# Optimization experiments

Measured on AMD Instinct MI355X. Metric: run time of the kernel, lower is better.

## Reference

```python
import jax, jax.numpy as jnp
import numpy as np

N_NODES = 50000

def cheb_conv(x, edge_index, W, b):
    # PyG ChebConv, K=2, normalization='sym', lambda_max=2.0 (default):
    # scaled Laplacian L_hat = (2/lambda_max)*L - I = -D^{-1/2} A D^{-1/2} (zero diag).
    # Tx_0 = x, Tx_1 = L_hat @ x ; out = Tx_0 @ W[0] + Tx_1 @ W[1] + b
    src, dst = edge_index[0], edge_index[1]
    ones = jnp.ones(src.shape[0], x.dtype)
    deg = jax.ops.segment_sum(ones, src, num_segments=N_NODES)
    dinv = jnp.where(deg > 0, 1.0 / jnp.sqrt(deg), 0.0)
    norm = -dinv[src] * dinv[dst]                                   # [E]
    tx1 = jax.ops.segment_sum(x[src] * norm[:, None], dst, num_segments=N_NODES)
    return x @ W[0] + tx1 @ W[1] + b

def setup_inputs() -> dict:
    key = jax.random.key(0)
    ks = jax.random.split(key, 12)
    IN, OUT, E, P = 128, 2, 800000, 400000
    return {
        "x": jax.random.normal(ks[0], (N_NODES, IN), jnp.float32),
        "edge_index": jax.random.randint(ks[1], (2, E), 0, N_NODES),
        "E_pos": jax.random.randint(ks[2], (2, P), 0, N_NODES),
        "neg_edge_index": jax.random.randint(ks[3], (2, P), 0, N_NODES),
        "W1": jax.random.normal(ks[4], (2, IN, 300), jnp.float32) * 0.05,
        "b1": jnp.zeros((300,), jnp.float32),
        "W2": jax.random.normal(ks[5], (2, 300, 100), jnp.float32) * 0.05,
        "b2": jnp.zeros((100,), jnp.float32),
        "W3": jax.random.normal(ks[6], (2, 100, OUT), jnp.float32) * 0.05,
        "b3": jnp.zeros((OUT,), jnp.float32),
        "lin1_W": jax.random.normal(ks[7], (100, IN), jnp.float32) * 0.05,
        "lin1_b": jnp.zeros((100,), jnp.float32),
        "lin2_W": jax.random.normal(ks[8], (100, IN), jnp.float32) * 0.05,
        "lin2_b": jnp.zeros((100,), jnp.float32),
        "c1": jnp.full((1,), 0.5, jnp.float32),
        "c2": jnp.full((1,), 0.5, jnp.float32),
    }

def reference(x, edge_index, E_pos, neg_edge_index, W1, b1, W2, b2, W3, b3,
              lin1_W, lin1_b, lin2_W, lin2_b, c1, c2):
    # eval mode: F.dropout and dropout_edge are identity
    x0 = x
    h = jax.nn.relu(cheb_conv(x0, edge_index, W1, b1))
    x1 = jax.nn.relu(cheb_conv(h, edge_index, W2, b2))
    x2 = x1 + jax.nn.relu(x0 @ lin1_W.T + lin1_b)
    z = x1 + jax.nn.relu(x0 @ lin2_W.T + lin2_b)
    pos_score = jnp.sum(z[E_pos[0]] * z[E_pos[1]], axis=1)              # [P]
    pos_loss = -jnp.mean(jnp.log(jax.nn.sigmoid(pos_score) + 1e-15))
    neg_score = jnp.sum(z[neg_edge_index[0]] * z[neg_edge_index[1]], axis=1)
    neg_loss = -jnp.mean(jnp.log(1.0 - jax.nn.sigmoid(neg_score) + 1e-15))
    r_loss = pos_loss + neg_loss
    out = cheb_conv(x2, edge_index, W3, b3)                             # [N, out_channels]
    return (out, r_loss, c1, c2)
```

## Files before the change

kernel.cpp:

```cpp
#include <hip/hip_runtime.h>
#include <math.h>


typedef unsigned short ushort_t;
typedef unsigned char u8;
typedef __attribute__((ext_vector_type(8))) __bf16 bf16x8;
typedef __attribute__((ext_vector_type(8))) short s16x8;
typedef __attribute__((ext_vector_type(4))) float f32x4;
typedef __attribute__((ext_vector_type(2))) float f32x2;

#define NB_H 64
#define HW 12500
#define PW 25000

__device__ __forceinline__ f32x4 mfma16x16x32(s16x8 a, s16x8 b, f32x4 c) {
  return __builtin_amdgcn_mfma_f32_16x16x32_bf16(
      __builtin_bit_cast(bf16x8, a), __builtin_bit_cast(bf16x8, b), c, 0, 0, 0);
}
__device__ __forceinline__ ushort_t f2bf(float f) {
  union { float f; unsigned u; } c; c.f = f;
  unsigned r = (c.u + 0x7FFFu + ((c.u >> 16) & 1u)) >> 16;
  return (ushort_t)r;
}
__device__ __forceinline__ f32x2 cvt2lo(unsigned u) {
  return __builtin_amdgcn_cvt_pk_f32_fp8((int)u, false);
}
__device__ __forceinline__ f32x2 cvt2hi(unsigned u) {
  return __builtin_amdgcn_cvt_pk_f32_fp8((int)u, true);
}
__device__ __forceinline__ u8 f2fp8(float f) {
  return (u8)(__builtin_amdgcn_cvt_pk_fp8_f32(f, 0.f, 0, false) & 0xff);
}

template<int VAR, int NT, int KTOT>
__global__ __launch_bounds__(256) void gemm_mfma(
    const ushort_t* __restrict__ A0, const ushort_t* __restrict__ A1,
    const ushort_t* __restrict__ Wt,
    const float* __restrict__ bias0, const float* __restrict__ bias1,
    const float* __restrict__ x1,
    const float* __restrict__ W3c, const float* __restrict__ b3c,
    void* __restrict__ out0, void* __restrict__ out1,
    float* __restrict__ t0g, float* __restrict__ t1g, int M)
{
  constexpr int NF = NT / 32;
  __shared__ __align__(16) ushort_t As[64 * 40];
  __shared__ __align__(16) ushort_t Bs[NT * 40];
  __shared__ float w3s[400];
  const int tid  = threadIdx.x;
  const int lane = tid & 63, w = tid >> 6;
  const int m0 = blockIdx.x * 64;
  const int wm = (w & 1) * 32, wn = (w >> 1) * (NT / 2);
  if (VAR == 2) { for (int i = tid; i < 400; i += 256) w3s[i] = W3c[i]; }
  f32x4 acc[2][NF];
#pragma unroll
  for (int i = 0; i < 2; ++i)
#pragma unroll
    for (int j = 0; j < NF; ++j) acc[i][j] = (f32x4){0.f, 0.f, 0.f, 0.f};

  for (int k0 = 0; k0 < KTOT; k0 += 32) {
    {
      const int r = tid >> 2, c8 = (tid & 3) * 8;
      const int gm = m0 + r;
      uint4 v = {0u, 0u, 0u, 0u};
      if (gm < M) {
        if (VAR == 1) {
          const u8* s8 = (const u8*)A0 + (size_t)gm * 320 + k0 + c8;
          const uint2 r8 = *(const uint2*)s8;
          const f32x2 f0 = cvt2lo(r8.x), f1 = cvt2hi(r8.x);
          const f32x2 f2 = cvt2lo(r8.y), f3 = cvt2hi(r8.y);
          v.x = (unsigned)f2bf(f0.x) | ((unsigned)f2bf(f0.y) << 16);
          v.y = (unsigned)f2bf(f1.x) | ((unsigned)f2bf(f1.y) << 16);
          v.z = (unsigned)f2bf(f2.x) | ((unsigned)f2bf(f2.y) << 16);
          v.w = (unsigned)f2bf(f3.x) | ((unsigned)f2bf(f3.y) << 16);
        } else {
          const ushort_t* srcp;
          if (VAR == 0) srcp = (k0 < 128) ? A0 + (size_t)gm * 128 + k0 + c8
                                          : A1 + (size_t)gm * 128 + (k0 - 128) + c8;
          else srcp = A0 + (size_t)gm * 128 + k0 + c8;
          v = *(const uint4*)srcp;
        }
      }
      *(uint4*)&As[r * 40 + c8] = v;
    }
    {
      const int c8 = (tid & 3) * 8;
#pragma unroll
      for (int i = 0; i < (NT * 4 + 255) / 256; ++i) {
        const int r = (tid >> 2) + i * 64;
        if (r < NT)
          *(uint4*)&Bs[r * 40 + c8] = *(const uint4*)(Wt + (size_t)r * KTOT + k0 + c8);
      }
    }
    __syncthreads();
    s16x8 af[2], bfr[NF];
#pragma unroll
    for (int mi = 0; mi < 2; ++mi)
      af[mi] = *(const s16x8*)&As[(wm + mi * 16 + (lane & 15)) * 40 + (lane >> 4) * 8];
#pragma unroll
    for (int ni = 0; ni < NF; ++ni)
      bfr[ni] = *(const s16x8*)&Bs[(wn + ni * 16 + (lane & 15)) * 40 + (lane >> 4) * 8];
#pragma unroll
    for (int mi = 0; mi < 2; ++mi)
#pragma unroll
      for (int ni = 0; ni < NF; ++ni)
        acc[mi][ni] = mfma16x16x32(af[mi], bfr[ni], acc[mi][ni]);
    __syncthreads();
  }

  if (VAR == 2) {
#pragma unroll
    for (int mi = 0; mi < 2; ++mi)
#pragma unroll
      for (int r = 0; r < 4; ++r) {
        const int gRow = m0 + wm + mi * 16 + ((lane >> 4) << 2) + r;
        float p0 = 0.f, p1 = 0.f, p2 = 0.f, p3 = 0.f;
#pragma unroll
        for (int ni = 0; ni < NF; ++ni) {
          const int col = wn + ni * 16 + (lane & 15);
          const float v = acc[mi][ni][r];
          if (gRow < M) {
            if (col < 100) {
              const float x2v = x1[(size_t)gRow * 128 + col] + fmaxf(v + bias0[col], 0.f);
              p0 = fmaf(x2v, w3s[col * 2 + 0], p0);
              p1 = fmaf(x2v, w3s[col * 2 + 1], p1);
              p2 = fmaf(x2v, w3s[200 + col * 2 + 0], p2);
              p3 = fmaf(x2v, w3s[200 + col * 2 + 1], p3);
            } else if (col < 200) {
              const int c = col - 100;
              ((u8*)out1)[(size_t)gRow * 128 + c] =
                  f2fp8(x1[(size_t)gRow * 128 + c] + fmaxf(v + bias1[c], 0.f));
            }
          }
        }
        if (wn == 0) {
#pragma unroll
          for (int off = 8; off; off >>= 1) {
            p0 += __shfl_down(p0, off, 16);
            p1 += __shfl_down(p1, off, 16);
            p2 += __shfl_down(p2, off, 16);
            p3 += __shfl_down(p3, off, 16);
          }
          if ((lane & 15) == 0 && gRow < M) {
            t0g[(size_t)gRow * 2 + 0] = p0 + b3c[0];
            t0g[(size_t)gRow * 2 + 1] = p1 + b3c[1];
            t1g[(size_t)gRow * 2 + 0] = p2;
            t1g[(size_t)gRow * 2 + 1] = p3;
          }
        }
      }
  } else {
#pragma unroll
    for (int mi = 0; mi < 2; ++mi)
#pragma unroll
      for (int ni = 0; ni < NF; ++ni)
#pragma unroll
        for (int r = 0; r < 4; ++r) {
          const int gRow = m0 + wm + mi * 16 + ((lane >> 4) << 2) + r;
          const int col  = wn + ni * 16 + (lane & 15);
          if (gRow >= M) continue;
          const float v = acc[mi][ni][r];
          if (VAR == 0) {
            ((u8*)out0)[(size_t)gRow * 320 + col] =
                (col < 300) ? f2fp8(fmaxf(v + bias0[col], 0.f)) : (u8)0;
          } else {
            if (col < 100) ((float*)out0)[(size_t)gRow * 128 + col] = v + bias0[col];
            else if (col < 200) ((u8*)out1)[(size_t)gRow * 128 + (col - 100)] = f2fp8(v);
          }
        }
  }
}

__global__ __launch_bounds__(256) void prep(
    const int* __restrict__ src, const int* __restrict__ dst, int E, int M,
    unsigned* __restrict__ partS, unsigned* __restrict__ partD,
    ushort_t* __restrict__ rank,
    const int* __restrict__ ep, const int* __restrict__ en, int P,
    unsigned* __restrict__ partP, ushort_t* __restrict__ prank,
    const float* __restrict__ x, ushort_t* __restrict__ xb,
    u8* __restrict__ xf8, int n4,
    const float* __restrict__ W1, const float* __restrict__ W2,
    const float* __restrict__ l1W, const float* __restrict__ l2W,
    ushort_t* __restrict__ W1t, ushort_t* __restrict__ W2t,
    ushort_t* __restrict__ Wlt)
{
  __shared__ unsigned hist[HW];
  const int blk = blockIdx.x;
  if (blk < 2 * NB_H) {
    const int isD = (blk >= NB_H);
    const int b = isD ? blk - NB_H : blk;
    const int* keys = isD ? dst : src;
    unsigned* part = isD ? partD : partS;
    const int cs = (E + NB_H - 1) / NB_H;
    const int e0 = b * cs;
    const int e1 = (e0 + cs < E) ? e0 + cs : E;
    for (int r = 0; r < 2; ++r) {
      const int klo = r * 2 * HW;
      for (int i = threadIdx.x; i < HW; i += 256) hist[i] = 0;
      __syncthreads();
      for (int e = e0 + threadIdx.x; e < e1; e += 256) {
        const int k = keys[e] - klo;
        if ((unsigned)k < (unsigned)(2 * HW)) {
          const unsigned old = atomicAdd(&hist[k >> 1], (k & 1) ? 0x10000u : 1u);
          if (isD) rank[e] = (ushort_t)((old >> ((k & 1) * 16)) & 0xffffu);
        }
      }
      __syncthreads();
      for (int i = threadIdx.x; i < HW; i += 256)
        part[(size_t)b * PW + r * HW + i] = hist[i];
      __syncthreads();
    }
    return;
  }
  if (blk < 3 * NB_H) {
    const int b = blk - 2 * NB_H;
    const int twoP = 2 * P;
    const int cs2 = (twoP + NB_H - 1) / NB_H;
    const int e0 = b * cs2;
    const int e1 = (e0 + cs2 < twoP) ? e0 + cs2 : twoP;
    for (int r = 0; r < 2; ++r) {
      const int klo = r * 2 * HW;
      for (int i = threadIdx.x; i < HW; i += 256) hist[i] = 0;
      __syncthreads();
      for (int i = e0 + threadIdx.x; i < e1; i += 256) {
        const int neg = (i >= P);
        const int p = neg ? i - P : i;
        const int* ia = neg ? en : ep;
        const int k = ia[p] - klo;
        if ((unsigned)k < (unsigned)(2 * HW)) {
          const unsigned old = atomicAdd(&hist[k >> 1], (k & 1) ? 0x10000u : 1u);
          prank[i] = (ushort_t)((old >> ((k & 1) * 16)) & 0xffffu);
        }
      }
      __syncthreads();
      for (int i = threadIdx.x; i < HW; i += 256)
        partP[(size_t)b * PW + r * HW + i] = hist[i];
      __syncthreads();
    }
    return;
  }
  const int i = (blk - 3 * NB_H) * 256 + threadIdx.x;
  if (i < n4) {
    const float4 v = ((const float4*)x)[i];
    ushort4 o; o.x = f2bf(v.x); o.y = f2bf(v.y); o.z = f2bf(v.z); o.w = f2bf(v.w);
    ((ushort4*)xb)[i] = o;
    int p = 0;
    p = __builtin_amdgcn_cvt_pk_fp8_f32(v.x, v.y, p, false);
    p = __builtin_amdgcn_cvt_pk_fp8_f32(v.z, v.w, p, true);
    ((unsigned*)xf8)[i] = (unsigned)p;
    return;
  }
  const int j = i - n4;
  if (j < 81920) {
    const int n = j >> 8, k = j & 255;
    float v = 0.f;
    if (n < 300) v = (k < 128) ? W1[k * 300 + n] : W1[38400 + (k - 128) * 300 + n];
    W1t[j] = f2bf(v);
  } else if (j < 153600) {
    const int jj = j - 81920;
    const int n = jj / 320, k = jj - n * 320;
    float v = 0.f;
    if (n < 200 && k < 300) v = W2[(n < 100 ? 0 : 30000) + k * 100 + (n % 100)];
    W2t[jj] = f2bf(v);
  } else if (j < 182272) {
    const int jj = j - 153600;
    const int n = jj >> 7, k = jj & 127;
    float v = 0.f;
    if (n < 100) v = l1W[n * 128 + k];
    else if (n < 200) v = l2W[(n - 100) * 128 + k];
    Wlt[jj] = f2bf(v);
  }
}

__global__ void scan_local(const unsigned* __restrict__ partS,
                           unsigned* __restrict__ partD,
                           unsigned* __restrict__ partP,
                           float* __restrict__ dinv,
                           int* __restrict__ ptr, int* __restrict__ pptr,
                           int* __restrict__ bsumE, int* __restrict__ bsumP, int n)
{
  __shared__ int tmp[256];
  const int i = blockIdx.x * 256 + threadIdx.x;
  const int lane = threadIdx.x & 63;
  unsigned ssum = 0, dtot = 0, ptot = 0;
  if (i < n && (i & 1) == 0) {
    const int c = i >> 1;
    for (int b = 0; b < NB_H; b += 8) {
      unsigned sv[8];
#pragma unroll
      for (int q = 0; q < 8; ++q) sv[q] = partS[(size_t)(b + q) * PW + c];
#pragma unroll
      for (int q = 0; q < 8; ++q) ssum += sv[q];
    }
    unsigned run = 0;
    for (int b = 0; b < NB_H; b += 8) {
      unsigned dv[8];
#pragma unroll
      for (int q = 0; q < 8; ++q) dv[q] = partD[(size_t)(b + q) * PW + c];
#pragma unroll
      for (int q = 0; q < 8; ++q) { const unsigned pre = run; run += dv[q]; dv[q] = pre; }
#pragma unroll
      for (int q = 0; q < 8; ++q) partD[(size_t)(b + q) * PW + c] = dv[q];
    }
    dtot = run;
    unsigned prun = 0;
    for (int b = 0; b < NB_H; b += 8) {
      unsigned pv[8];
#pragma unroll
      for (int q = 0; q < 8; ++q) pv[q] = partP[(size_t)(b + q) * PW + c];
#pragma unroll
      for (int q = 0; q < 8; ++q) { const unsigned pre = prun; prun += pv[q]; pv[q] = pre; }
#pragma unroll
      for (int q = 0; q < 8; ++q) partP[(size_t)(b + q) * PW + c] = pv[q];
    }
    ptot = prun;
  }
  const unsigned sAll = __shfl(ssum, lane & ~1, 64);
  const unsigned dAll = __shfl(dtot, lane & ~1, 64);
  const unsigned pAll = __shfl(ptot, lane & ~1, 64);
  int v = 0, v2 = 0;
  if (i < n) {
    const int hs = (i & 1) * 16;
    const unsigned dg = (sAll >> hs) & 0xffffu;
    dinv[i] = dg ? 1.f / sqrtf((float)dg) : 0.f;
    v = (int)((dAll >> hs) & 0xffffu);
    v2 = (int)((pAll >> hs) & 0xffffu);
  }
  tmp[threadIdx.x] = v;
  __syncthreads();
  for (int off = 1; off < 256; off <<= 1) {
    const int t = (threadIdx.x >= off) ? tmp[threadIdx.x - off] : 0;
    __syncthreads();
    tmp[threadIdx.x] += t;
    __syncthreads();
  }
  if (i < n) ptr[i] = tmp[threadIdx.x] - v;
  if (threadIdx.x == 255) bsumE[blockIdx.x] = tmp[255];
  __syncthreads();
  tmp[threadIdx.x] = v2;
  __syncthreads();
  for (int off = 1; off < 256; off <<= 1) {
    const int t = (threadIdx.x >= off) ? tmp[threadIdx.x - off] : 0;
    __syncthreads();
    tmp[threadIdx.x] += t;
    __syncthreads();
  }
  if (i < n) pptr[i] = tmp[threadIdx.x] - v2;
  if (threadIdx.x == 255) bsumP[blockIdx.x] = tmp[255];
}

__global__ void scan_add2(int* __restrict__ ptr, int* __restrict__ pptr,
                          const int* __restrict__ bsumE, const int* __restrict__ bsumP,
                          int n, int E, int twoP, int nb, float* __restrict__ accs)
{
  __shared__ int tmp[256];
  const int v = (threadIdx.x < nb) ? bsumE[threadIdx.x] : 0;
  tmp[threadIdx.x] = v;
  __syncthreads();
  for (int off = 1; off < 256; off <<= 1) {
    const int t = (threadIdx.x >= off) ? tmp[threadIdx.x - off] : 0;
    __syncthreads();
    tmp[threadIdx.x] += t;
    __syncthreads();
  }
  const int offE = (blockIdx.x > 0) ? tmp[blockIdx.x - 1] : 0;
  __syncthreads();
  const int v2 = (threadIdx.x < nb) ? bsumP[threadIdx.x] : 0;
  tmp[threadIdx.x] = v2;
  __syncthreads();
  for (int off = 1; off < 256; off <<= 1) {
    const int t = (threadIdx.x >= off) ? tmp[threadIdx.x - off] : 0;
    __syncthreads();
    tmp[threadIdx.x] += t;
    __syncthreads();
  }
  const int offP = (blockIdx.x > 0) ? tmp[blockIdx.x - 1] : 0;
  const int i = blockIdx.x * 256 + threadIdx.x;
  if (i < n) { ptr[i] += offE; pptr[i] += offP; }
  if (i == 0) { ptr[n] = E; pptr[n] = twoP; accs[0] = 0.f; accs[1] = 0.f; }
}

__global__ __launch_bounds__(256) void fill2(
    const int* __restrict__ src, const int* __restrict__ dst,
    const float* __restrict__ dinv, const int* __restrict__ ptr,
    const unsigned* __restrict__ baseD, const ushort_t* __restrict__ rank,
    int2* __restrict__ csr, int E, int fillE,
    const int* __restrict__ ep, const int* __restrict__ en, int P,
    const int* __restrict__ pptr, const unsigned* __restrict__ baseP,
    const ushort_t* __restrict__ prank, int* __restrict__ pnb)
{
  const int blk = blockIdx.x;
  if (blk < fillE) {
    const int e = blk * 256 + threadIdx.x;
    if (e >= E) return;
    const int cs = (E + NB_H - 1) / NB_H;
    const int b = e / cs;
    const int s = src[e], d = dst[e];
    const unsigned bv = baseD[(size_t)b * PW + (d >> 1)];
    const int base = (int)((bv >> ((d & 1) * 16)) & 0xffffu);
    const int pos = ptr[d] + base + (int)rank[e];
    const float w = -dinv[s] * dinv[d];
    csr[pos] = make_int2(s, __float_as_int(w));
    return;
  }
  const int i = (blk - fillE) * 256 + threadIdx.x;
  const int twoP = 2 * P;
  if (i >= twoP) return;
  const int neg = (i >= P);
  const int p = neg ? i - P : i;
  const int* ia = neg ? en : ep;
  const int na = ia[p], nbv = ia[P + p];
  const int cs2 = (twoP + NB_H - 1) / NB_H;
  const int b = i / cs2;
  const unsigned bv = baseP[(size_t)b * PW + (na >> 1)];
  const int base = (int)((bv >> ((na & 1) * 16)) & 0xffffu);
  const int pos = pptr[na] + base + (int)prank[i];
  pnb[pos] = nbv | (neg ? (int)0x80000000 : 0);
}

#define ACCV(u, ww) { f32x2 t; \
  t = cvt2lo(u.x); a[0]  = fmaf(ww, t.x, a[0]);  a[1]  = fmaf(ww, t.y, a[1]);  \
  t = cvt2hi(u.x); a[2]  = fmaf(ww, t.x, a[2]);  a[3]  = fmaf(ww, t.y, a[3]);  \
  t = cvt2lo(u.y); a[4]  = fmaf(ww, t.x, a[4]);  a[5]  = fmaf(ww, t.y, a[5]);  \
  t = cvt2hi(u.y); a[6]  = fmaf(ww, t.x, a[6]);  a[7]  = fmaf(ww, t.y, a[7]);  \
  t = cvt2lo(u.z); a[8]  = fmaf(ww, t.x, a[8]);  a[9]  = fmaf(ww, t.y, a[9]);  \
  t = cvt2hi(u.z); a[10] = fmaf(ww, t.x, a[10]); a[11] = fmaf(ww, t.y, a[11]); \
  t = cvt2lo(u.w); a[12] = fmaf(ww, t.x, a[12]); a[13] = fmaf(ww, t.y, a[13]); \
  t = cvt2hi(u.w); a[14] = fmaf(ww, t.x, a[14]); a[15] = fmaf(ww, t.y, a[15]); }

__global__ __launch_bounds__(256) void gather128e(
    const u8* __restrict__ xf8, ushort_t* __restrict__ txb,
    const int* __restrict__ ptr, const int2* __restrict__ csr, int M)
{
  const int node = (blockIdx.x * 256 + threadIdx.x) >> 3;
  const int sub  = threadIdx.x & 7;
  if (node >= M) return;
  const int beg = ptr[node], end = ptr[node + 1];
  float a[16] = {};
  int p = beg;
  for (; p + 8 <= end; p += 8) {
    int2 e[8];
#pragma unroll
    for (int q = 0; q < 8; ++q) e[q] = csr[p + q];
    uint4 v[8];
#pragma unroll
    for (int q = 0; q < 8; ++q)
      v[q] = *(const uint4*)(xf8 + (size_t)e[q].x * 128 + sub * 16);
#pragma unroll
    for (int q = 0; q < 8; ++q) { const float wq = __int_as_float(e[q].y); ACCV(v[q], wq) }
  }
  for (; p < end; ++p) {
    const int2 eq = csr[p]; const float wq = __int_as_float(eq.y);
    const uint4 v = *(const uint4*)(xf8 + (size_t)eq.x * 128 + sub * 16);
    ACCV(v, wq)
  }
  uint4 o1, o2;
  o1.x = (unsigned)f2bf(a[0])  | ((unsigned)f2bf(a[1])  << 16);
  o1.y = (unsigned)f2bf(a[2])  | ((unsigned)f2bf(a[3])  << 16);
  o1.z = (unsigned)f2bf(a[4])  | ((unsigned)f2bf(a[5])  << 16);
  o1.w = (unsigned)f2bf(a[6])  | ((unsigned)f2bf(a[7])  << 16);
  o2.x = (unsigned)f2bf(a[8])  | ((unsigned)f2bf(a[9])  << 16);
  o2.y = (unsigned)f2bf(a[10]) | ((unsigned)f2bf(a[11]) << 16);
  o2.z = (unsigned)f2bf(a[12]) | ((unsigned)f2bf(a[13]) << 16);
  o2.w = (unsigned)f2bf(a[14]) | ((unsigned)f2bf(a[15]) << 16);
  ushort_t* dstp = txb + (size_t)node * 128 + sub * 16;
  *(uint4*)dstp = o1;
  *(uint4*)(dstp + 8) = o2;
}

__global__ __launch_bounds__(256) void gather100e_x1(
    const u8* __restrict__ Brh, float* __restrict__ Ar,
    const int* __restrict__ ptr, const int2* __restrict__ csr, int M)
{
  const int node = (blockIdx.x * 256 + threadIdx.x) >> 3;
  const int sub  = threadIdx.x & 7;
  if (node >= M) return;
  const int beg = ptr[node], end = ptr[node + 1];
  float a[16] = {};
  int p = beg;
  for (; p + 8 <= end; p += 8) {
    int2 e[8];
#pragma unroll
    for (int q = 0; q < 8; ++q) e[q] = csr[p + q];
    uint4 v[8];
#pragma unroll
    for (int q = 0; q < 8; ++q)
      v[q] = *(const uint4*)(Brh + (size_t)e[q].x * 128 + sub * 16);
#pragma unroll
    for (int q = 0; q < 8; ++q) { const float wq = __int_as_float(e[q].y); ACCV(v[q], wq) }
  }
  for (; p < end; ++p) {
    const int2 eq = csr[p]; const float wq = __int_as_float(eq.y);
    const uint4 v = *(const uint4*)(Brh + (size_t)eq.x * 128 + sub * 16);
    ACCV(v, wq)
  }
  float* dstp = Ar + (size_t)node * 128 + sub * 16;
#pragma unroll
  for (int q = 0; q < 4; ++q) {
    float4 b = *(const float4*)(dstp + q * 4);
    b.x = fmaxf(b.x + a[q * 4 + 0], 0.f);
    b.y = fmaxf(b.y + a[q * 4 + 1], 0.f);
    b.z = fmaxf(b.z + a[q * 4 + 2], 0.f);
    b.w = fmaxf(b.w + a[q * 4 + 3], 0.f);
    *(float4*)(dstp + q * 4) = b;
  }
}
#undef ACCV

__device__ __forceinline__ void maskrow(uint4& r, int sub) {
  if (sub >= 6) { r.y = 0u; r.z = 0u; r.w = 0u; if (sub == 7) r.x = 0u; }
}
#define DOTA(vv, s) { f32x2 q_; \
  q_ = cvt2lo(vv.x); s = fmaf(af[0],  q_.x, s); s = fmaf(af[1],  q_.y, s); \
  q_ = cvt2hi(vv.x); s = fmaf(af[2],  q_.x, s); s = fmaf(af[3],  q_.y, s); \
  q_ = cvt2lo(vv.y); s = fmaf(af[4],  q_.x, s); s = fmaf(af[5],  q_.y, s); \
  q_ = cvt2hi(vv.y); s = fmaf(af[6],  q_.x, s); s = fmaf(af[7],  q_.y, s); \
  q_ = cvt2lo(vv.z); s = fmaf(af[8],  q_.x, s); s = fmaf(af[9],  q_.y, s); \
  q_ = cvt2hi(vv.z); s = fmaf(af[10], q_.x, s); s = fmaf(af[11], q_.y, s); \
  q_ = cvt2lo(vv.w); s = fmaf(af[12], q_.x, s); s = fmaf(af[13], q_.y, s); \
  q_ = cvt2hi(vv.w); s = fmaf(af[14], q_.x, s); s = fmaf(af[15], q_.y, s); }

__global__ __launch_bounds__(256) void loss_g2(
    const u8* __restrict__ zf8, const int* __restrict__ pptr,
    const int* __restrict__ pnb, float* __restrict__ acc,
    const float* __restrict__ t1, const float* __restrict__ t0,
    const int* __restrict__ ptr, const int2* __restrict__ csr,
    float* __restrict__ out, int M, int lossNB)
{
  const int tid = threadIdx.x;
  if (blockIdx.x >= lossNB) {
    const int i = (blockIdx.x - lossNB) * 256 + tid;
    if (i >= M) return;
    float a0 = 0.f, a1 = 0.f;
    const int beg = ptr[i], end = ptr[i + 1];
    int p = beg;
    for (; p + 4 <= end; p += 4) {
      const int2 e0 = csr[p], e1 = csr[p + 1], e2 = csr[p + 2], e3 = csr[p + 3];
      const float w0 = __int_as_float(e0.y), w1 = __int_as_float(e1.y);
      const float w2 = __int_as_float(e2.y), w3 = __int_as_float(e3.y);
      const float2 v0 = *(const float2*)(t1 + (size_t)e0.x * 2);
      const float2 v1 = *(const float2*)(t1 + (size_t)e1.x * 2);
      const float2 v2 = *(const float2*)(t1 + (size_t)e2.x * 2);
      const float2 v3 = *(const float2*)(t1 + (size_t)e3.x * 2);
      a0 = fmaf(w0, v0.x, a0); a1 = fmaf(w0, v0.y, a1);
      a0 = fmaf(w1, v1.x, a0); a1 = fmaf(w1, v1.y, a1);
      a0 = fmaf(w2, v2.x, a0); a1 = fmaf(w2, v2.y, a1);
      a0 = fmaf(w3, v3.x, a0); a1 = fmaf(w3, v3.y, a1);
    }
    for (; p < end; ++p) {
      const int2 eq = csr[p]; const float wq = __int_as_float(eq.y);
      const float2 v = *(const float2*)(t1 + (size_t)eq.x * 2);
      a0 = fmaf(wq, v.x, a0); a1 = fmaf(wq, v.y, a1);
    }
    const float2 base = *(const float2*)(t0 + (size_t)i * 2);
    *(float2*)(out + (size_t)i * 2) = make_float2(base.x + a0, base.y + a1);
    return;
  }
  __shared__ float red[8];
  const int lane = tid & 63, wib = tid >> 6;
  const int sub = tid & 7;
  const int node = (blockIdx.x * 256 + tid) >> 3;
  float tp = 0.f, tn = 0.f;
  if (node < M) {
    uint4 ra = make_uint4(0u, 0u, 0u, 0u);
    if (sub < 7) ra = *(const uint4*)(zf8 + (size_t)node * 128 + sub * 16);
    maskrow(ra, sub);
    float af[16];
    { f32x2 t;
      t = cvt2lo(ra.x); af[0]  = t.x; af[1]  = t.y;
      t = cvt2hi(ra.x); af[2]  = t.x; af[3]  = t.y;
      t = cvt2lo(ra.y); af[4]  = t.x; af[5]  = t.y;
      t = cvt2hi(ra.y); af[6]  = t.x; af[7]  = t.y;
      t = cvt2lo(ra.z); af[8]  = t.x; af[9]  = t.y;
      t = cvt2hi(ra.z); af[10] = t.x; af[11] = t.y;
      t = cvt2lo(ra.w); af[12] = t.x; af[13] = t.y;
      t = cvt2hi(ra.w); af[14] = t.x; af[15] = t.y; }
    const int beg = pptr[node], end = pptr[node + 1];
    int p = beg;
    for (; p + 4 <= end; p += 4) {
      int nb4[4];
#pragma unroll
      for (int q = 0; q < 4; ++q) nb4[q] = pnb[p + q];
      uint4 rb[4];
#pragma unroll
      for (int q = 0; q < 4; ++q) {
        rb[q] = make_uint4(0u, 0u, 0u, 0u);
        const int nv = nb4[q] & 0x7fffffff;
        if (sub < 7) rb[q] = *(const uint4*)(zf8 + (size_t)nv * 128 + sub * 16);
        maskrow(rb[q], sub);
      }
      float s[4] = {0.f, 0.f, 0.f, 0.f};
#pragma unroll
      for (int q = 0; q < 4; ++q) DOTA(rb[q], s[q])
#pragma unroll
      for (int off = 4; off; off >>= 1) {
#pragma unroll
        for (int q = 0; q < 4; ++q) s[q] += __shfl_down(s[q], off, 8);
      }
      if (sub == 0) {
#pragma unroll
        for (int q = 0; q < 4; ++q) {
          const float sig = 1.f / (1.f + __expf(-s[q]));
          if ((unsigned)nb4[q] >> 31) tn += __logf(1.f - sig + 1e-15f);
          else tp += __logf(sig + 1e-15f);
        }
      }
    }
    for (; p < end; ++p) {
      const int nbv = pnb[p];
      const int nv = nbv & 0x7fffffff;
      uint4 rb = make_uint4(0u, 0u, 0u, 0u);
      if (sub < 7) rb = *(const uint4*)(zf8 + (size_t)nv * 128 + sub * 16);
      maskrow(rb, sub);
      float s = 0.f;
      DOTA(rb, s)
#pragma unroll
      for (int off = 4; off; off >>= 1) s += __shfl_down(s, off, 8);
      if (sub == 0) {
        const float sig = 1.f / (1.f + __expf(-s));
        if ((unsigned)nbv >> 31) tn += __logf(1.f - sig + 1e-15f);
        else tp += __logf(sig + 1e-15f);
      }
    }
  }
  tp += __shfl_down(tp, 32, 64); tn += __shfl_down(tn, 32, 64);
  tp += __shfl_down(tp, 16, 64); tn += __shfl_down(tn, 16, 64);
  tp += __shfl_down(tp, 8, 64);  tn += __shfl_down(tn, 8, 64);
  if (lane == 0) { red[wib] = tp; red[4 + wib] = tn; }
  __syncthreads();
  if (tid == 0) {
    atomicAdd(acc + 0, red[0] + red[1] + red[2] + red[3]);
    atomicAdd(acc + 1, red[4] + red[5] + red[6] + red[7]);
  }
}
#undef DOTA

__global__ void final_scalars(const float* __restrict__ accs,
                              const float* __restrict__ c1, const float* __restrict__ c2,
                              float* __restrict__ out, int M, float invP)
{
  out[2 * M + 0] = -(accs[0] + accs[1]) * invP;
  out[2 * M + 1] = c1[0];
  out[2 * M + 2] = c2[0];
}

extern "C" void kernel_launch(void* const* d_in, const int* in_sizes, int n_in,
                              void* d_out, int out_size, void* d_ws, size_t ws_size,
                              hipStream_t stream)
{
  const float* x   = (const float*)d_in[0];
  const int*   ei  = (const int*)d_in[1];
  const int*   ep  = (const int*)d_in[2];
  const int*   en  = (const int*)d_in[3];
  const float* W1  = (const float*)d_in[4];
  const float* b1  = (const float*)d_in[5];
  const float* W2  = (const float*)d_in[6];
  const float* b2  = (const float*)d_in[7];
  const float* W3  = (const float*)d_in[8];
  const float* b3  = (const float*)d_in[9];
  const float* l1W = (const float*)d_in[10];
  const float* l1b = (const float*)d_in[11];
  const float* l2W = (const float*)d_in[12];
  const float* l2b = (const float*)d_in[13];
  const float* c1  = (const float*)d_in[14];
  const float* c2  = (const float*)d_in[15];
  float* out = (float*)d_out;

  const int M = in_sizes[0] / 128;
  const int E = in_sizes[1] / 2;
  const int P = in_sizes[2] / 2;
  const int* src = ei;
  const int* dst = ei + E;
  const int nb_scan = (M + 255) / 256;
  const int fillE = (E + 255) / 256;
  const int fillP = (2 * P + 255) / 256;
  const int lossNB = (M * 8 + 255) / 256;

  float* ws = (float*)d_ws;
  size_t o = 0;
  float*    dinv = ws + o;            o += 50176;
  int*      ptr  = (int*)(ws + o);    o += (size_t)M + 8;
  int*      pptr = (int*)(ws + o);    o += (size_t)M + 8;
  int*      bsumE = (int*)(ws + o);   o += 256;
  int*      bsumP = (int*)(ws + o);   o += 256;
  int2*     csr  = (int2*)(ws + o);   o += (size_t)E * 2;
  ushort_t* rank = (ushort_t*)(ws + o); o += (size_t)E / 2;
  int*      pnb  = (int*)(ws + o);    o += (size_t)2 * P;
  ushort_t* xb   = (ushort_t*)(ws + o); o += (size_t)M * 64;
  u8*       xf8  = (u8*)(ws + o);     o += (size_t)M * 32;
  ushort_t* tx0b = (ushort_t*)(ws + o); o += (size_t)M * 64;
  ushort_t* W1t  = (ushort_t*)(ws + o); o += 40960;
  ushort_t* W2t  = (ushort_t*)(ws + o); o += 35840;
  ushort_t* Wlt  = (ushort_t*)(ws + o); o += 14336;
  u8*       h8   = (u8*)(ws + o);     o += (size_t)M * 160;
  float*    Ar   = ws + o;            o += (size_t)M * 128;
  u8*       Brh  = (u8*)(ws + o);     o += (size_t)M * 32;
  u8*       zf8  = (u8*)(ws + o);     o += (size_t)M * 32;
  float*    t0   = ws + o;            o += (size_t)M * 2;
  float*    t1   = ws + o;            o += (size_t)M * 2;
  float*    accs = ws + o;            o += 8;
  unsigned* partS = (unsigned*)h8;
  unsigned* partD = (unsigned*)Ar;
  ushort_t* prank = tx0b;
  unsigned* partP = (unsigned*)((char*)tx0b + (size_t)2 * P * 2);

  const int n4 = M * 32;
  const int packBlocks = (n4 + 182272 + 255) / 256;
  prep<<<3 * NB_H + packBlocks, 256, 0, stream>>>(
      src, dst, E, M, partS, partD, rank,
      ep, en, P, partP, prank,
      x, xb, xf8, n4, W1, W2, l1W, l2W, W1t, W2t, Wlt);

  scan_local<<<nb_scan, 256, 0, stream>>>(partS, partD, partP, dinv, ptr, pptr,
                                          bsumE, bsumP, M);
  scan_add2<<<nb_scan, 256, 0, stream>>>(ptr, pptr, bsumE, bsumP, M, E, 2 * P,
                                         nb_scan, accs);
  fill2<<<fillE + fillP, 256, 0, stream>>>(
      src, dst, dinv, ptr, partD, rank, csr, E, fillE,
      ep, en, P, pptr, partP, prank, pnb);

  const int gB = (M + 63) / 64;
  const int gE8 = (M * 8 + 255) / 256;

  gather128e<<<gE8, 256, 0, stream>>>(xf8, tx0b, ptr, csr, M);
  gemm_mfma<0, 320, 256><<<gB, 256, 0, stream>>>(
      xb, tx0b, W1t, b1, nullptr, nullptr, nullptr, nullptr, h8, nullptr, nullptr, nullptr, M);

  gemm_mfma<1, 224, 320><<<gB, 256, 0, stream>>>(
      (const ushort_t*)h8, nullptr, W2t, b2, nullptr, nullptr, nullptr, nullptr,
      Ar, Brh, nullptr, nullptr, M);
  gather100e_x1<<<gE8, 256, 0, stream>>>(Brh, Ar, ptr, csr, M);

  gemm_mfma<2, 224, 128><<<gB, 256, 0, stream>>>(
      xb, nullptr, Wlt, l1b, l2b, Ar , W3, b3, nullptr, zf8, t0, t1, M);

  loss_g2<<<lossNB + nb_scan, 256, 0, stream>>>(
      zf8, pptr, pnb, accs, t1, t0, ptr, csr, out, M, lossNB);
  final_scalars<<<1, 1, 0, stream>>>(accs, c1, c2, out, M, 1.0f / (float)P);
}
```

Baseline: 457.3 us.

## Move pair-CSR fill into first GEMM launch and reorder loss block roles

Splits the combined edge/pair fill kernel. The positive/negative pair scatter now runs as extra tail blocks of the first MFMA GEMM launch, so it overlaps with GEMM work instead of sitting on the critical path before the gather. The partP and prank scratch buffers move from tx0b, which that GEMM reads, into the Ar region to avoid aliasing. In the loss kernel the output-SpMM blocks are now scheduled first, ahead of the loss blocks. This relies on Ar not being written before the first GEMM finishes, and adds a branch to the GEMM kernel.

```diff
diff --git a/kernel.cpp b/kernel.cpp
--- a/kernel.cpp
+++ b/kernel.cpp
@@ -40,8 +40,28 @@
     const float* __restrict__ x1,
     const float* __restrict__ W3c, const float* __restrict__ b3c,
     void* __restrict__ out0, void* __restrict__ out1,
-    float* __restrict__ t0g, float* __restrict__ t1g, int M)
-{
+    float* __restrict__ t0g, float* __restrict__ t1g, int M,
+    int gemmNB,
+    const int* __restrict__ ep, const int* __restrict__ en, int P,
+    const int* __restrict__ pptr, const unsigned* __restrict__ baseP,
+    const ushort_t* __restrict__ prank, int* __restrict__ pnb)
+{
+  if (VAR == 0 && (int)blockIdx.x >= gemmNB) {
+    const int i = ((int)blockIdx.x - gemmNB) * 256 + (int)threadIdx.x;
+    const int twoP = 2 * P;
+    if (i >= twoP) return;
+    const int neg = (i >= P);
+    const int p = neg ? i - P : i;
+    const int* ia = neg ? en : ep;
+    const int na = ia[p], nbv = ia[P + p];
+    const int cs2 = (twoP + NB_H - 1) / NB_H;
+    const int b = i / cs2;
+    const unsigned bv = baseP[(size_t)b * PW + (na >> 1)];
+    const int base = (int)((bv >> ((na & 1) * 16)) & 0xffffu);
+    const int pos = pptr[na] + base + (int)prank[i];
+    pnb[pos] = nbv | (neg ? (int)0x80000000 : 0);
+    return;
+  }
   constexpr int NF = NT / 32;
   __shared__ __align__(16) ushort_t As[64 * 40];
   __shared__ __align__(16) ushort_t Bs[NT * 40];
@@ -379,42 +399,22 @@
   if (i == 0) { ptr[n] = E; pptr[n] = twoP; accs[0] = 0.f; accs[1] = 0.f; }
 }
 
-__global__ __launch_bounds__(256) void fill2(
-    const int* __restrict__ src, const int* __restrict__ dst,
-    const float* __restrict__ dinv, const int* __restrict__ ptr,
-    const unsigned* __restrict__ baseD, const ushort_t* __restrict__ rank,
-    int2* __restrict__ csr, int E, int fillE,
-    const int* __restrict__ ep, const int* __restrict__ en, int P,
-    const int* __restrict__ pptr, const unsigned* __restrict__ baseP,
-    const ushort_t* __restrict__ prank, int* __restrict__ pnb)
-{
-  const int blk = blockIdx.x;
-  if (blk < fillE) {
-    const int e = blk * 256 + threadIdx.x;
-    if (e >= E) return;
-    const int cs = (E + NB_H - 1) / NB_H;
-    const int b = e / cs;
-    const int s = src[e], d = dst[e];
-    const unsigned bv = baseD[(size_t)b * PW + (d >> 1)];
-    const int base = (int)((bv >> ((d & 1) * 16)) & 0xffffu);
-    const int pos = ptr[d] + base + (int)rank[e];
-    const float w = -dinv[s] * dinv[d];
-    csr[pos] = make_int2(s, __float_as_int(w));
-    return;
-  }
-  const int i = (blk - fillE) * 256 + threadIdx.x;
-  const int twoP = 2 * P;
-  if (i >= twoP) return;
-  const int neg = (i >= P);
-  const int p = neg ? i - P : i;
-  const int* ia = neg ? en : ep;
-  const int na = ia[p], nbv = ia[P + p];
-  const int cs2 = (twoP + NB_H - 1) / NB_H;
-  const int b = i / cs2;
-  const unsigned bv = baseP[(size_t)b * PW + (na >> 1)];
-  const int base = (int)((bv >> ((na & 1) * 16)) & 0xffffu);
-  const int pos = pptr[na] + base + (int)prank[i];
-  pnb[pos] = nbv | (neg ? (int)0x80000000 : 0);
+__global__ void fill_csr2(const int* __restrict__ src, const int* __restrict__ dst,
+                          const float* __restrict__ dinv, const int* __restrict__ ptr,
+                          const unsigned* __restrict__ baseD,
+                          const ushort_t* __restrict__ rank,
+                          int2* __restrict__ csr, int E)
+{
+  const int e = blockIdx.x * 256 + threadIdx.x;
+  if (e >= E) return;
+  const int cs = (E + NB_H - 1) / NB_H;
+  const int b = e / cs;
+  const int s = src[e], d = dst[e];
+  const unsigned bv = baseD[(size_t)b * PW + (d >> 1)];
+  const int base = (int)((bv >> ((d & 1) * 16)) & 0xffffu);
+  const int pos = ptr[d] + base + (int)rank[e];
+  const float w = -dinv[s] * dinv[d];
+  csr[pos] = make_int2(s, __float_as_int(w));
 }
 
 #define ACCV(u, ww) { f32x2 t; \
@@ -524,11 +524,11 @@
     const int* __restrict__ pnb, float* __restrict__ acc,
     const float* __restrict__ t1, const float* __restrict__ t0,
     const int* __restrict__ ptr, const int2* __restrict__ csr,
-    float* __restrict__ out, int M, int lossNB)
+    float* __restrict__ out, int M, int nbScan)
 {
   const int tid = threadIdx.x;
-  if (blockIdx.x >= lossNB) {
-    const int i = (blockIdx.x - lossNB) * 256 + tid;
+  if ((int)blockIdx.x < nbScan) {
+    const int i = blockIdx.x * 256 + tid;
     if (i >= M) return;
     float a0 = 0.f, a1 = 0.f;
     const int beg = ptr[i], end = ptr[i + 1];
@@ -558,7 +558,7 @@
   __shared__ float red[8];
   const int lane = tid & 63, wib = tid >> 6;
   const int sub = tid & 7;
-  const int node = (blockIdx.x * 256 + tid) >> 3;
+  const int node = (((int)blockIdx.x - nbScan) * 256 + tid) >> 3;
   float tp = 0.f, tn = 0.f;
   if (node < M) {
     uint4 ra = make_uint4(0u, 0u, 0u, 0u);
@@ -700,8 +700,8 @@
   float*    accs = ws + o;            o += 8;
   unsigned* partS = (unsigned*)h8;
   unsigned* partD = (unsigned*)Ar;
-  ushort_t* prank = tx0b;
-  unsigned* partP = (unsigned*)((char*)tx0b + (size_t)2 * P * 2);
+  unsigned* partP = (unsigned*)Ar + 1600000;
+  ushort_t* prank = (ushort_t*)((unsigned*)Ar + 3200000);
 
   const int n4 = M * 32;
   const int packBlocks = (n4 + 182272 + 255) / 256;
@@ -714,26 +714,27 @@
                                           bsumE, bsumP, M);
   scan_add2<<<nb_scan, 256, 0, stream>>>(ptr, pptr, bsumE, bsumP, M, E, 2 * P,
                                          nb_scan, accs);
-  fill2<<<fillE + fillP, 256, 0, stream>>>(
-      src, dst, dinv, ptr, partD, rank, csr, E, fillE,
-      ep, en, P, pptr, partP, prank, pnb);
+  fill_csr2<<<fillE, 256, 0, stream>>>(src, dst, dinv, ptr, partD, rank, csr, E);
 
   const int gB = (M + 63) / 64;
   const int gE8 = (M * 8 + 255) / 256;
 
   gather128e<<<gE8, 256, 0, stream>>>(xf8, tx0b, ptr, csr, M);
-  gemm_mfma<0, 320, 256><<<gB, 256, 0, stream>>>(
-      xb, tx0b, W1t, b1, nullptr, nullptr, nullptr, nullptr, h8, nullptr, nullptr, nullptr, M);
+  gemm_mfma<0, 320, 256><<<gB + fillP, 256, 0, stream>>>(
+      xb, tx0b, W1t, b1, nullptr, nullptr, nullptr, nullptr, h8, nullptr,
+      nullptr, nullptr, M, gB, ep, en, P, pptr, partP, prank, pnb);
 
   gemm_mfma<1, 224, 320><<<gB, 256, 0, stream>>>(
       (const ushort_t*)h8, nullptr, W2t, b2, nullptr, nullptr, nullptr, nullptr,
-      Ar, Brh, nullptr, nullptr, M);
+      Ar, Brh, nullptr, nullptr, M, gB, nullptr, nullptr, 0, nullptr, nullptr,
+      nullptr, nullptr);
   gather100e_x1<<<gE8, 256, 0, stream>>>(Brh, Ar, ptr, csr, M);
 
   gemm_mfma<2, 224, 128><<<gB, 256, 0, stream>>>(
-      xb, nullptr, Wlt, l1b, l2b, Ar , W3, b3, nullptr, zf8, t0, t1, M);
-
-  loss_g2<<<lossNB + nb_scan, 256, 0, stream>>>(
-      zf8, pptr, pnb, accs, t1, t0, ptr, csr, out, M, lossNB);
+      xb, nullptr, Wlt, l1b, l2b, Ar , W3, b3, nullptr, zf8, t0, t1, M,
+      gB, nullptr, nullptr, 0, nullptr, nullptr, nullptr, nullptr);
+
+  loss_g2<<<nb_scan + lossNB, 256, 0, stream>>>(
+      zf8, pptr, pnb, accs, t1, t0, ptr, csr, out, M, nb_scan);
   final_scalars<<<1, 1, 0, stream>>>(accs, c1, c2, out, M, 1.0f / (float)P);
 }
```

Result: no change. 454.6 us (-0.6%).
